# Kernel optimization log

Hardware: AMD Instinct MI355X
Metric: run time of the kernel (lower is better)

Reference implementation:

```python
import jax, jax.numpy as jnp
import numpy as np

B, T, C = 2, 4096, 2048
HS = 64
H = C // HS            # 32 heads
D_W, D_A, D_MV, D_G = 128, 128, 64, 224
EPS_GN = 0.00064
EPS_NORM = 1e-12


def setup_inputs() -> dict:
    key = jax.random.key(0)
    ks = jax.random.split(key, 24)
    n = lambda k, s, sc=1.0: (jax.random.normal(k, s, dtype=jnp.float32) * sc)
    inp = {
        "x": n(ks[0], (B, T, C)),
        "v_first": n(ks[1], (B, T, C)),
        "y": n(ks[2], (B, T, C)),
        # token-shift mixing coefficients [1,1,C]
        "x_r": n(ks[3], (1, 1, C), 0.1), "x_w": n(ks[4], (1, 1, C), 0.1),
        "x_k": n(ks[5], (1, 1, C), 0.1), "x_v": n(ks[6], (1, 1, C), 0.1),
        "x_a": n(ks[7], (1, 1, C), 0.1), "x_g": n(ks[8], (1, 1, C), 0.1),
        # decay LoRA
        "w0": n(ks[9], (1, 1, C), 0.5) - 3.0,
        "w1": n(ks[10], (C, D_W), 0.02), "w2": n(ks[11], (D_W, C), 0.02),
        # in-context-rate LoRA
        "a0": n(ks[12], (1, 1, C), 0.2),
        "a1": n(ks[13], (C, D_A), 0.02), "a2": n(ks[14], (D_A, C), 0.02),
        # value-mix LoRA
        "v0": n(ks[15], (1, 1, C), 0.2) + 0.73,
        "v1": n(ks[16], (C, D_MV), 0.02), "v2": n(ks[17], (D_MV, C), 0.02),
        # gate LoRA
        "g1": n(ks[18], (C, D_G), 0.02), "g2": n(ks[19], (D_G, C), 0.02),
        "k_k": jnp.full((1, 1, C), 0.71, dtype=jnp.float32),
        "k_a": jnp.full((1, 1, C), 1.02, dtype=jnp.float32),
        "r_k": jnp.full((H, HS), -0.04, dtype=jnp.float32),
        # square projections
        "W_r": n(ks[20], (C, C), 0.5 / C ** 0.5),
        "W_k": n(ks[21], (C, C), 0.05 / C ** 0.5),
        "W_v": n(ks[22], (C, C), 0.5 / C ** 0.5),
        "W_o": n(ks[23], (C, C), 0.02),
        "ln_g": jnp.ones((C,), dtype=jnp.float32),
        "ln_b": jnp.zeros((C,), dtype=jnp.float32),
    }
    return inp


def reference(x, v_first, y, x_r, x_w, x_k, x_v, x_a, x_g,
              w0, w1, w2, a0, a1, a2, v0, v1, v2, g1, g2,
              k_k, k_a, r_k, W_r, W_k, W_v, W_o, ln_g, ln_b):
    Bx, Tx, Cx = x.shape
    Hn, hs = r_k.shape

    # ---- project ----
    xx = jnp.pad(x[:, :-1, :], ((0, 0), (1, 0), (0, 0))) - x  # time_shift_1(x) - x
    xr = x + xx * x_r
    xw = x + xx * x_w
    xk = x + xx * x_k
    xv = x + xx * x_v
    xa = x + xx * x_a
    xg = x + xx * x_g

    r = xr @ W_r.T
    w = -jax.nn.softplus(-(w0 + jnp.tanh(xw @ w1) @ w2)) - 0.5
    k = xk @ W_k.T
    v = xv @ W_v.T
    # layer_id == 1 (> 0): mix with v_first
    v = v + (v_first - v) * jax.nn.sigmoid(v0 + (xv @ v1) @ v2)
    a = jax.nn.sigmoid(a0 + (xa @ a1) @ a2)
    g = jax.nn.sigmoid(xg @ g1) @ g2

    kk = k * k_k
    kkh = kk.reshape(Bx, Tx, Hn, hs)
    nrm = jnp.sqrt(jnp.sum(kkh * kkh, axis=-1, keepdims=True))
    kk = (kkh / jnp.maximum(nrm, EPS_NORM)).reshape(Bx, Tx, Cx)
    k = k * (1.0 + (a - 1.0) * k_a)

    # ---- post_kernel ----
    yh = y.reshape(Bx, Tx, Hn, hs)
    mu = jnp.mean(yh, axis=-1, keepdims=True)
    var = jnp.mean((yh - mu) ** 2, axis=-1, keepdims=True)
    yn = ((yh - mu) / jnp.sqrt(var + EPS_GN)).reshape(Bx, Tx, Cx)
    yn = yn * ln_g + ln_b

    rh = r.reshape(Bx, Tx, Hn, hs)
    kh = k.reshape(Bx, Tx, Hn, hs)
    vh = v.reshape(Bx, Tx, Hn, hs)
    dot = jnp.sum(rh * kh * r_k, axis=-1, keepdims=True)  # [B,T,H,1]
    y2 = yn + (dot * vh).reshape(Bx, Tx, Cx)
    out = (y2 * g) @ W_o.T
    return out, w, a, kk
```

## Files before the change

kernel.cpp:

```cpp
#include <hip/hip_runtime.h>
#include <math.h>

typedef unsigned short u16;
typedef __attribute__((ext_vector_type(8))) short short8;
typedef __attribute__((ext_vector_type(4))) float floatx4;
typedef __attribute__((ext_vector_type(4))) unsigned short ushort4v;
typedef __attribute__((ext_vector_type(8))) unsigned short ushort8v;

#define DEV static __device__ __forceinline__

DEV u16 f2b(float f) {
  unsigned u = __builtin_bit_cast(unsigned, f);
  u += 0x7fffu + ((u >> 16) & 1u);
  return (u16)(u >> 16);
}
DEV float b2f(u16 h) { return __builtin_bit_cast(float, ((unsigned)h) << 16); }

DEV void gld16(const u16* g, u16* l) {
  __builtin_amdgcn_global_load_lds((__attribute__((address_space(1))) void*)(g),
                                   (__attribute__((address_space(3))) void*)(l), 16, 0, 0);
}

__global__ __launch_bounds__(256) void ew_mix(
    const float* __restrict__ x,
    const float* __restrict__ cr, const float* __restrict__ ck,
    const float* __restrict__ cv, const float* __restrict__ cw,
    const float* __restrict__ ca, const float* __restrict__ cg,
    u16* __restrict__ oxr, u16* __restrict__ oxk, u16* __restrict__ oxv,
    u16* __restrict__ oxw, u16* __restrict__ oxa, u16* __restrict__ oxg)
{
  const long idx = (long)blockIdx.x * 256 + threadIdx.x;
  const long row = idx >> 8;
  const int c8 = (int)(idx & 255) << 3;
  const long off = (row << 11) + c8;
  const floatx4 xa_ = *(const floatx4*)(x + off);
  const floatx4 xb_ = *(const floatx4*)(x + off + 4);
  floatx4 pa = (floatx4)0.f, pb = (floatx4)0.f;
  if ((row & 4095) != 0) {
    pa = *(const floatx4*)(x + off - 2048);
    pb = *(const floatx4*)(x + off - 2044);
  }
  floatx4 da, db;
#pragma unroll
  for (int i = 0; i < 4; ++i) { da[i] = pa[i] - xa_[i]; db[i] = pb[i] - xb_[i]; }
#define EMIT(cp, op) {                                                         \
    const floatx4 c0 = *(const floatx4*)(cp + c8);                             \
    const floatx4 c1 = *(const floatx4*)(cp + c8 + 4);                         \
    ushort8v o;                                                                \
    _Pragma("unroll")                                                          \
    for (int i = 0; i < 4; ++i) {                                              \
      o[i]     = f2b(xa_[i] + da[i] * c0[i]);                                  \
      o[4 + i] = f2b(xb_[i] + db[i] * c1[i]);                                  \
    }                                                                          \
    *(ushort8v*)(op + off) = o; }
  EMIT(cr, oxr); EMIT(ck, oxk); EMIT(cv, oxv);
  EMIT(cw, oxw); EMIT(ca, oxa); EMIT(cg, oxg);
#undef EMIT
}

__global__ __launch_bounds__(256) void transpose_cast(
    const float* __restrict__ w1, const float* __restrict__ a1,
    const float* __restrict__ v1, const float* __restrict__ g1,
    const float* __restrict__ w2, const float* __restrict__ a2,
    const float* __restrict__ v2, const float* __restrict__ g2,
    u16* __restrict__ w1T, u16* __restrict__ a1T, u16* __restrict__ v1T,
    u16* __restrict__ g1T, u16* __restrict__ w2T, u16* __restrict__ a2T,
    u16* __restrict__ v2T, u16* __restrict__ g2T,
    const float* __restrict__ Wr, const float* __restrict__ Wk,
    const float* __restrict__ Wv, const float* __restrict__ Wo,
    u16* __restrict__ Wr16, u16* __restrict__ Wk16,
    u16* __restrict__ Wv16, u16* __restrict__ Wo16)
{
  const long idx = (long)blockIdx.x * 256 + threadIdx.x;
  if (blockIdx.y >= 8) {
    const float* s; u16* d;
    switch (blockIdx.y) {
      case 8:  s = Wr; d = Wr16; break;
      case 9:  s = Wk; d = Wk16; break;
      case 10: s = Wv; d = Wv16; break;
      default: s = Wo; d = Wo16; break;
    }
    const long i = idx * 8;
    const float4 a = *(const float4*)(s + i);
    const float4 b = *(const float4*)(s + i + 4);
    ushort4v lo = { f2b(a.x), f2b(a.y), f2b(a.z), f2b(a.w) };
    ushort4v hi = { f2b(b.x), f2b(b.y), f2b(b.z), f2b(b.w) };
    *(ushort4v*)(d + i) = lo;
    *(ushort4v*)(d + i + 4) = hi;
    return;
  }
  const float* src; u16* dst; int sk, sn, dn, dk;
  switch (blockIdx.y) {
    case 0: src = w1; dst = w1T; sk = 2048; sn = 128; dn = 128;  dk = 2048; break;
    case 1: src = a1; dst = a1T; sk = 2048; sn = 128; dn = 128;  dk = 2048; break;
    case 2: src = v1; dst = v1T; sk = 2048; sn = 64;  dn = 128;  dk = 2048; break;
    case 3: src = g1; dst = g1T; sk = 2048; sn = 224; dn = 256;  dk = 2048; break;
    case 4: src = w2; dst = w2T; sk = 128;  sn = 2048; dn = 2048; dk = 128; break;
    case 5: src = a2; dst = a2T; sk = 128;  sn = 2048; dn = 2048; dk = 128; break;
    case 6: src = v2; dst = v2T; sk = 64;   sn = 2048; dn = 2048; dk = 128; break;
    default:src = g2; dst = g2T; sk = 224;  sn = 2048; dn = 2048; dk = 256; break;
  }
  const long total = (long)dn * dk;
  if (idx >= total) return;
  const int n = (int)(idx / dk), k = (int)(idx % dk);
  float v = 0.f;
  if (k < sk && n < sn) v = src[(long)k * sn + n];
  dst[idx] = f2b(v);
}

#define GEMM128_BODY(Abase, Bbase, K)                                          \
  floatx4 acc[4][4];                                                           \
  _Pragma("unroll")                                                            \
  for (int i = 0; i < 4; ++i)                                                  \
    _Pragma("unroll")                                                          \
    for (int jq = 0; jq < 4; ++jq) acc[i][jq] = (floatx4)0.f;                  \
  const int nK = (K) >> 6;                                                     \
  for (int kt = 0; kt < nK; ++kt) {                                            \
    const int k0 = kt << 6;                                                    \
    __syncthreads();                                                           \
    _Pragma("unroll")                                                          \
    for (int i = 0; i < 4; ++i) {                                              \
      const int c = i * 256 + tid;                                             \
      const int row = c >> 3;                                                  \
      const int sch = (c & 7) ^ (row & 7);                                     \
      const long goff = (long)row * (K) + k0 + sch * 8;                        \
      const int lbase = (i * 256 + wave * 64) * 8;                             \
      gld16((Abase) + goff, &sA[lbase]);                                       \
      gld16((Bbase) + goff, &sB[lbase]);                                       \
    }                                                                          \
    asm volatile("s_waitcnt vmcnt(0)" ::: "memory");                           \
    __syncthreads();                                                           \
    _Pragma("unroll")                                                          \
    for (int ks = 0; ks < 2; ++ks) {                                           \
      short8 af[4], bfr[4];                                                    \
      _Pragma("unroll")                                                        \
      for (int mi = 0; mi < 4; ++mi) {                                         \
        const int row = wm * 64 + mi * 16 + lrow;                              \
        const int ch = (ks * 4 + lkg) ^ (row & 7);                             \
        af[mi] = *(const short8*)&sA[row * 64 + ch * 8];                       \
      }                                                                        \
      _Pragma("unroll")                                                        \
      for (int ni = 0; ni < 4; ++ni) {                                         \
        const int row = wn * 64 + ni * 16 + lrow;                              \
        const int ch = (ks * 4 + lkg) ^ (row & 7);                             \
        bfr[ni] = *(const short8*)&sB[row * 64 + ch * 8];                      \
      }                                                                        \
      _Pragma("unroll")                                                        \
      for (int mi = 0; mi < 4; ++mi)                                           \
        _Pragma("unroll")                                                      \
        for (int ni = 0; ni < 4; ++ni)                                         \
          acc[mi][ni] = __builtin_amdgcn_mfma_f32_16x16x32_bf16(af[mi], bfr[ni], acc[mi][ni], 0, 0, 0); \
    }                                                                          \
  }

__global__ __launch_bounds__(256, 2) void gemm_s1(
    const u16* __restrict__ xw, const u16* __restrict__ w1T, u16* __restrict__ hw,
    const u16* __restrict__ xa, const u16* __restrict__ a1T, u16* __restrict__ ha,
    const u16* __restrict__ xv, const u16* __restrict__ v1T, u16* __restrict__ hv,
    const u16* __restrict__ xg, const u16* __restrict__ g1T, u16* __restrict__ hg)
{
  __shared__ __align__(16) u16 sA[128 * 64];
  __shared__ __align__(16) u16 sB[128 * 64];
  const int bid = blockIdx.x;
  const int jid = (bid < 64) ? 0 : (bid < 128) ? 1 : (bid < 192) ? 2 : 3;
  const u16* A = (jid == 0) ? xw : (jid == 1) ? xa : (jid == 2) ? xv : xg;
  const u16* B = (jid == 0) ? w1T : (jid == 1) ? a1T : (jid == 2) ? v1T : g1T;
  u16* Cv = (jid == 0) ? hw : (jid == 1) ? ha : (jid == 2) ? hv : hg;
  const int N = (jid == 3) ? 256 : 128;
  const int lb = bid - ((jid == 0) ? 0 : (jid == 1) ? 64 : (jid == 2) ? 128 : 192);
  const int tid = threadIdx.x;
  const int wave = tid >> 6, lane = tid & 63;
  const int lrow = lane & 15, lkg = lane >> 4;
  const int wm = wave >> 1, wn = wave & 1;
  const int nbn = N >> 7;
  const int bm = lb / nbn, bn = lb % nbn;
  const u16* Abase = A + (long)bm * 128 * 2048;
  const u16* Bbase = B + (long)bn * 128 * 2048;

  GEMM128_BODY(Abase, Bbase, 2048)

  const int row0 = bm * 128 + wm * 64 + lkg * 4;
  const int col0 = bn * 128 + wn * 64 + lrow;
#pragma unroll
  for (int mi = 0; mi < 4; ++mi)
#pragma unroll
    for (int ni = 0; ni < 4; ++ni) {
      const int col = col0 + ni * 16;
#pragma unroll
      for (int r = 0; r < 4; ++r) {
        const long o = (long)(row0 + mi * 16 + r) * N + col;
        float v = acc[mi][ni][r];
        if (jid == 0) v = tanhf(v);
        else if (jid == 3) v = 1.f / (1.f + expf(-v));
        Cv[o] = f2b(v);
      }
    }
}

__global__ __launch_bounds__(256, 2) void gemm_s2(
    const u16* __restrict__ hw, const u16* __restrict__ w2T, float* __restrict__ wsec, const float* __restrict__ w0,
    const u16* __restrict__ ha, const u16* __restrict__ a2T, float* __restrict__ asec, const float* __restrict__ a0,
    const u16* __restrict__ hv, const u16* __restrict__ v2T, u16* __restrict__ vs, const float* __restrict__ v0,
    const u16* __restrict__ hg, const u16* __restrict__ g2T, u16* __restrict__ gb)
{
  __shared__ __align__(16) u16 sA[128 * 64];
  __shared__ __align__(16) u16 sB[128 * 64];
  const int jid = blockIdx.x >> 10;
  const int lb = blockIdx.x & 1023;
  const u16* A = (jid == 0) ? hw : (jid == 1) ? ha : (jid == 2) ? hv : hg;
  const u16* B = (jid == 0) ? w2T : (jid == 1) ? a2T : (jid == 2) ? v2T : g2T;
  const float* bias = (jid == 0) ? w0 : (jid == 1) ? a0 : v0;
  const int K = (jid == 3) ? 256 : 128;
  const int tid = threadIdx.x;
  const int wave = tid >> 6, lane = tid & 63;
  const int lrow = lane & 15, lkg = lane >> 4;
  const int wm = wave >> 1, wn = wave & 1;
  const int bm = lb >> 4, bn = lb & 15;
  const u16* Abase = A + (long)bm * 128 * K;
  const u16* Bbase = B + (long)bn * 128 * K;

  GEMM128_BODY(Abase, Bbase, K)

  const int row0 = bm * 128 + wm * 64 + lkg * 4;
  const int col0 = bn * 128 + wn * 64 + lrow;
#pragma unroll
  for (int mi = 0; mi < 4; ++mi)
#pragma unroll
    for (int ni = 0; ni < 4; ++ni) {
      const int col = col0 + ni * 16;
#pragma unroll
      for (int r = 0; r < 4; ++r) {
        const long o = (long)(row0 + mi * 16 + r) * 2048 + col;
        const float v = acc[mi][ni][r];
        if (jid == 0) {
          const float zz = -(v + bias[col]);
          const float sp = fmaxf(zz, 0.f) + log1pf(expf(-fabsf(zz)));
          wsec[o] = -sp - 0.5f;
        } else if (jid == 1) {
          asec[o] = 1.f / (1.f + expf(-(v + bias[col])));
        } else if (jid == 2) {
          vs[o] = f2b(1.f / (1.f + expf(-(v + bias[col]))));
        } else {
          gb[o] = f2b(v);
        }
      }
    }
}

template<int OP>
__global__ __launch_bounds__(512, 2) void gemm256(
    const u16* __restrict__ A0, const u16* __restrict__ B0, void* __restrict__ C0,
    const u16* __restrict__ A1, const u16* __restrict__ B1, void* __restrict__ C1,
    const u16* __restrict__ A2, const u16* __restrict__ B2, void* __restrict__ C2)
{
  __shared__ __align__(16) u16 lds[8 * 8192];
  const int tid = threadIdx.x;
  const int wave = tid >> 6, lane = tid & 63;
  const int lrow = lane & 15, lq = lane >> 4;
  const int wm = wave >> 2, wn = wave & 3;
  const int job = blockIdx.x >> 8;
  const int d = blockIdx.x & 255;
  const int lb = ((d & 7) << 5) | (d >> 3);
  const int bm = lb >> 3, bn = lb & 7;

  const u16* Aj = (job == 0) ? A0 : ((job == 1) ? A1 : A2);
  const u16* Bj = (job == 0) ? B0 : ((job == 1) ? B1 : B2);
  void* Cj      = (job == 0) ? C0 : ((job == 1) ? C1 : C2);

  const u16* __restrict__ Ab = Aj + (long)bm * 256 * 2048;
  const u16* __restrict__ Bb = Bj + (long)bn * 256 * 2048;

  int srco[2], dsto[2];
#pragma unroll
  for (int l = 0; l < 2; ++l) {
    const int c = l * 512 + tid;
    const int row = c >> 2, q = c & 3;
    const int qs = q ^ ((row >> 1) & 3);
    srco[l] = row * 2048 + qs * 8;
    dsto[l] = (l * 512 + wave * 64) * 8;
  }
  int offA[2][4], offB[4];
#pragma unroll
  for (int qm = 0; qm < 2; ++qm)
#pragma unroll
    for (int mi = 0; mi < 4; ++mi) {
      const int r = wm * 128 + qm * 64 + mi * 16 + lrow;
      offA[qm][mi] = r * 32 + (lq ^ ((r >> 1) & 3)) * 8;
    }
#pragma unroll
  for (int ni = 0; ni < 4; ++ni) {
    const int r = wn * 64 + ni * 16 + lrow;
    offB[ni] = r * 32 + (lq ^ ((r >> 1) & 3)) * 8;
  }

  floatx4 acc[8][4];
#pragma unroll
  for (int i = 0; i < 8; ++i)
#pragma unroll
    for (int jq = 0; jq < 4; ++jq) acc[i][jq] = (floatx4)0.f;

#define STAGE(sU, slot) {                                                  \
    const int t_ = (sU) >> 2, j_ = (sU) & 3;                               \
    const u16* base_ = (j_ & 1) ? Bb : Ab;                                 \
    const int kofs_ = t_ * 64 + ((j_ & 2) ? 32 : 0);                       \
    gld16(base_ + srco[0] + kofs_, &lds[(slot) * 8192 + dsto[0]]);         \
    gld16(base_ + srco[1] + kofs_, &lds[(slot) * 8192 + dsto[1]]);         \
  }

#pragma unroll
  for (int s = 0; s < 6; ++s) STAGE(s, s);
  asm volatile("s_waitcnt vmcnt(4)" ::: "memory");

#define SEC(P, sA_, sB_, sS0, sS1)                                             \
  {                                                                            \
    asm volatile("s_barrier" ::: "memory");                                    \
    if ((P) <= 60) {                                                           \
      STAGE(2 * (P) + 6, sS0);                                                 \
      STAGE(2 * (P) + 7, sS1);                                                 \
    }                                                                          \
    short8 af0[4], af1[4], bfv[4];                                             \
    _Pragma("unroll")                                                          \
    for (int mi = 0; mi < 4; ++mi)                                             \
      af0[mi] = *(const short8*)&lds[(sA_) * 8192 + offA[0][mi]];              \
    _Pragma("unroll")                                                          \
    for (int ni = 0; ni < 4; ++ni)                                             \
      bfv[ni] = *(const short8*)&lds[(sB_) * 8192 + offB[ni]];                 \
    _Pragma("unroll")                                                          \
    for (int mi = 0; mi < 4; ++mi)                                             \
      af1[mi] = *(const short8*)&lds[(sA_) * 8192 + offA[1][mi]];              \
    _Pragma("unroll")                                                          \
    for (int mi = 0; mi < 4; ++mi)                                             \
      _Pragma("unroll")                                                        \
      for (int ni = 0; ni < 4; ++ni)                                           \
        acc[mi][ni] = __builtin_amdgcn_mfma_f32_16x16x32_bf16(af0[mi], bfv[ni], acc[mi][ni], 0, 0, 0); \
    _Pragma("unroll")                                                          \
    for (int mi = 0; mi < 4; ++mi)                                             \
      _Pragma("unroll")                                                        \
      for (int ni = 0; ni < 4; ++ni)                                           \
        acc[4 + mi][ni] = __builtin_amdgcn_mfma_f32_16x16x32_bf16(af1[mi], bfv[ni], acc[4 + mi][ni], 0, 0, 0); \
    if ((P) < 62) { asm volatile("s_waitcnt vmcnt(4)" ::: "memory"); }         \
    else          { asm volatile("s_waitcnt vmcnt(0)" ::: "memory"); }         \
  }

  for (int pp = 0; pp < 64; pp += 4) {
    SEC(pp,     0, 1, 6, 7);
    SEC(pp + 1, 2, 3, 0, 1);
    SEC(pp + 2, 4, 5, 2, 3);
    SEC(pp + 3, 6, 7, 4, 5);
  }
#undef SEC
#undef STAGE

  const long row0 = (long)bm * 256 + wm * 128 + lq * 4;
  const int col0 = bn * 256 + wn * 64 + lrow;
#pragma unroll
  for (int mi = 0; mi < 8; ++mi) {
#pragma unroll
    for (int ni = 0; ni < 4; ++ni) {
      const int col = col0 + ni * 16;
#pragma unroll
      for (int r = 0; r < 4; ++r) {
        const long o = (row0 + mi * 16 + r) * 2048 + col;
        const float v = acc[mi][ni][r];
        if constexpr (OP == 0) ((float*)Cj)[o] = v;
        else ((u16*)Cj)[o] = f2b(v);
      }
    }
  }
}

DEV float wsum16(float v) {
  v += __shfl_xor(v, 1);  v += __shfl_xor(v, 2);
  v += __shfl_xor(v, 4);  v += __shfl_xor(v, 8);
  return v;
}

__global__ __launch_bounds__(256) void ew_head(
    const u16* __restrict__ r16, const u16* __restrict__ k16,
    float* __restrict__ kkout,
    const float* __restrict__ abuf,
    const u16* __restrict__ v0buf, const u16* __restrict__ vsbuf,
    const u16* __restrict__ gbuf,
    const float* __restrict__ y, const float* __restrict__ vfirst,
    const float* __restrict__ kkc, const float* __restrict__ kac,
    const float* __restrict__ rk, const float* __restrict__ lng,
    const float* __restrict__ lnb, u16* __restrict__ z)
{
  const int tid = threadIdx.x;
  const long gh = (long)blockIdx.x * 16 + (tid >> 4);
  const long m = gh >> 5;
  const int h = (int)(gh & 31);
  const int li = tid & 15;
  const int c = h * 64 + li * 4;
  const long off = (m << 11) + c;

  const ushort4v k0p = *(const ushort4v*)(k16 + off);
  const floatx4 av   = *(const floatx4*)(abuf + off);
  const floatx4 kkcv = *(const floatx4*)(kkc + c);
  const floatx4 kacv = *(const floatx4*)(kac + c);
  float k0[4], kf[4], kr[4];
  float ss = 0.f;
#pragma unroll
  for (int i = 0; i < 4; ++i) {
    k0[i] = b2f(k0p[i]);
    kf[i] = k0[i] * (1.f + (av[i] - 1.f) * kacv[i]);
    kr[i] = k0[i] * kkcv[i];
    ss += kr[i] * kr[i];
  }
  const float nrm = sqrtf(wsum16(ss));
  const float rn = 1.f / fmaxf(nrm, 1e-12f);
  floatx4 kkv;
#pragma unroll
  for (int i = 0; i < 4; ++i) kkv[i] = kr[i] * rn;
  *(floatx4*)(kkout + off) = kkv;

  const floatx4 yv = *(const floatx4*)(y + off);
  const float mu = wsum16(yv[0] + yv[1] + yv[2] + yv[3]) * 0.015625f;
  float dy[4], sv2 = 0.f;
#pragma unroll
  for (int i = 0; i < 4; ++i) { dy[i] = yv[i] - mu; sv2 += dy[i] * dy[i]; }
  const float var = wsum16(sv2) * 0.015625f;
  const float rs = rsqrtf(var + 0.00064f);
  const floatx4 lngv = *(const floatx4*)(lng + c);
  const floatx4 lnbv = *(const floatx4*)(lnb + c);
  float yn[4];
#pragma unroll
  for (int i = 0; i < 4; ++i) yn[i] = dy[i] * rs * lngv[i] + lnbv[i];

  const ushort4v rp = *(const ushort4v*)(r16 + off);
  const floatx4 rkv = *(const floatx4*)(rk + c);
  float dd = 0.f;
#pragma unroll
  for (int i = 0; i < 4; ++i) dd += b2f(rp[i]) * kf[i] * rkv[i];
  const float dot = wsum16(dd);

  const ushort4v v0p = *(const ushort4v*)(v0buf + off);
  const ushort4v vsp = *(const ushort4v*)(vsbuf + off);
  const floatx4 vfv  = *(const floatx4*)(vfirst + off);
  const ushort4v gp  = *(const ushort4v*)(gbuf + off);
  ushort4v zo;
#pragma unroll
  for (int i = 0; i < 4; ++i) {
    const float v0v = b2f(v0p[i]);
    const float vv = v0v + (vfv[i] - v0v) * b2f(vsp[i]);
    zo[i] = f2b((yn[i] + dot * vv) * b2f(gp[i]));
  }
  *(ushort4v*)(z + off) = zo;
}

extern "C" void kernel_launch(void* const* d_in, const int* in_sizes, int n_in,
                              void* d_out, int out_size, void* d_ws, size_t ws_size,
                              hipStream_t stream)
{
  (void)in_sizes; (void)out_size;
  if (n_in < 29) return;
  const int Mrows = 8192;
  const long C = 2048;
  const long MB_ = (long)Mrows * C;

  const float* x   = (const float*)d_in[0];
  const float* vf  = (const float*)d_in[1];
  const float* y   = (const float*)d_in[2];
  const float* x_r = (const float*)d_in[3];
  const float* x_w = (const float*)d_in[4];
  const float* x_k = (const float*)d_in[5];
  const float* x_v = (const float*)d_in[6];
  const float* x_a = (const float*)d_in[7];
  const float* x_g = (const float*)d_in[8];
  const float* w0  = (const float*)d_in[9];
  const float* w1  = (const float*)d_in[10];
  const float* w2  = (const float*)d_in[11];
  const float* a0  = (const float*)d_in[12];
  const float* a1  = (const float*)d_in[13];
  const float* a2  = (const float*)d_in[14];
  const float* v0  = (const float*)d_in[15];
  const float* v1  = (const float*)d_in[16];
  const float* v2  = (const float*)d_in[17];
  const float* g1  = (const float*)d_in[18];
  const float* g2  = (const float*)d_in[19];
  const float* k_k = (const float*)d_in[20];
  const float* k_a = (const float*)d_in[21];
  const float* r_k = (const float*)d_in[22];
  const float* W_r = (const float*)d_in[23];
  const float* W_k = (const float*)d_in[24];
  const float* W_v = (const float*)d_in[25];
  const float* W_o = (const float*)d_in[26];
  const float* lng = (const float*)d_in[27];
  const float* lnb = (const float*)d_in[28];

  float* out_sec = (float*)d_out;
  float* w_sec   = out_sec + MB_;
  float* a_sec   = w_sec + MB_;
  float* kk_sec  = a_sec + MB_;

  u16* k16 = (u16*)out_sec;
  u16* r16 = (u16*)out_sec + MB_;
  u16* Wr16 = (u16*)w_sec;
  u16* Wk16 = Wr16 + C * C;
  u16* Wv16 = Wk16 + C * C;

  u16* p = (u16*)d_ws;
  u16* xr = p;            p += MB_;
  u16* xk = p;            p += MB_;
  u16* xv = p;            p += MB_;
  u16* xw = p;            p += MB_;
  u16* xa = p;            p += MB_;
  u16* xg = p;            p += MB_;
  u16* Wo16 = p;          p += C * C;
  u16* w1T = p;           p += 128 * C;
  u16* a1T = p;           p += 128 * C;
  u16* v1T = p;           p += 128 * C;
  u16* g1T = p;           p += 256 * C;
  u16* w2T = p;           p += C * 128;
  u16* a2T = p;           p += C * 128;
  u16* v2T = p;           p += C * 128;
  u16* g2T = p;           p += C * 256;
  u16* hw  = p;           p += (long)Mrows * 128;
  u16* ha  = p;           p += (long)Mrows * 128;
  u16* hv  = p;           p += (long)Mrows * 128;
  u16* hg  = p;           p += (long)Mrows * 256;
  const size_t need = (size_t)((char*)p - (char*)d_ws);
  if (ws_size < need) return;

  u16* v0buf = xg;
  u16* zbuf  = xk;
  u16* vsbuf = xw;
  u16* gbuf  = xa;

  ew_mix<<<8192, 256, 0, stream>>>(x, x_r, x_k, x_v, x_w, x_a, x_g,
                                   xr, xk, xv, xw, xa, xg);
  transpose_cast<<<dim3(2048, 12), 256, 0, stream>>>(
      w1, a1, v1, g1, w2, a2, v2, g2,
      w1T, a1T, v1T, g1T, w2T, a2T, v2T, g2T,
      W_r, W_k, W_v, W_o, Wr16, Wk16, Wv16, Wo16);
  gemm_s1<<<320, 256, 0, stream>>>(xw, w1T, hw, xa, a1T, ha,
                                   xv, v1T, hv, xg, g1T, hg);
  gemm256<1><<<768, 512, 0, stream>>>(xr, Wr16, r16,
                                      xk, Wk16, k16,
                                      xv, Wv16, v0buf);
  gemm_s2<<<4096, 256, 0, stream>>>(hw, w2T, w_sec, w0,
                                    ha, a2T, a_sec, a0,
                                    hv, v2T, vsbuf, v0,
                                    hg, g2T, gbuf);
  ew_head<<<16384, 256, 0, stream>>>(r16, k16, kk_sec, a_sec, v0buf, vsbuf, gbuf,
                                     y, vf, k_k, k_a, r_k, lng, lnb, zbuf);
  gemm256<0><<<256, 512, 0, stream>>>(zbuf, Wo16, out_sec,
                                      zbuf, Wo16, out_sec,
                                      zbuf, Wo16, out_sec);
}
```

Measured before the change: 672.2 us.

## Fuse LoRA second-stage GEMMs with head elementwise epilogue into one kernel

Replaces the separate gemm_s2 kernel and the ew_head elementwise kernel with a single s2_head kernel. Each block runs the a, v, g and w LoRA up-projections for the same 128x128 output tile back to back, keeping a, the value-mix sigmoid and the gate in registers as packed bf16. It then does the key normalisation, group norm, r·k dot and z computation in place. This removes the global round trips for the vs and g intermediates and the re-read of a, plus one kernel launch. In exchange it raises register pressure from the extra packed tiles and cuts the grid from 4096 blocks to 1024. It also uses scalar, less vectorised loads in the epilogue.

Result: slower. 704.5 us (+4.8%).

```diff
diff --git a/kernel.cpp b/kernel.cpp
--- a/kernel.cpp
+++ b/kernel.cpp
@@ -110,46 +110,51 @@
 
 #define GEMM128_BODY(Abase, Bbase, K)                                          \
   floatx4 acc[4][4];                                                           \
+  GEMM128_RUN(Abase, Bbase, K)
+
+#define GEMM128_RUN(Abase, Bbase, K)                                           \
   _Pragma("unroll")                                                            \
   for (int i = 0; i < 4; ++i)                                                  \
     _Pragma("unroll")                                                          \
     for (int jq = 0; jq < 4; ++jq) acc[i][jq] = (floatx4)0.f;                  \
-  const int nK = (K) >> 6;                                                     \
-  for (int kt = 0; kt < nK; ++kt) {                                            \
-    const int k0 = kt << 6;                                                    \
-    __syncthreads();                                                           \
-    _Pragma("unroll")                                                          \
-    for (int i = 0; i < 4; ++i) {                                              \
-      const int c = i * 256 + tid;                                             \
-      const int row = c >> 3;                                                  \
-      const int sch = (c & 7) ^ (row & 7);                                     \
-      const long goff = (long)row * (K) + k0 + sch * 8;                        \
-      const int lbase = (i * 256 + wave * 64) * 8;                             \
-      gld16((Abase) + goff, &sA[lbase]);                                       \
-      gld16((Bbase) + goff, &sB[lbase]);                                       \
-    }                                                                          \
-    asm volatile("s_waitcnt vmcnt(0)" ::: "memory");                           \
-    __syncthreads();                                                           \
-    _Pragma("unroll")                                                          \
-    for (int ks = 0; ks < 2; ++ks) {                                           \
-      short8 af[4], bfr[4];                                                    \
+  {                                                                            \
+    const int nK = (K) >> 6;                                                   \
+    for (int kt = 0; kt < nK; ++kt) {                                          \
+      const int kk0 = kt << 6;                                                 \
+      __syncthreads();                                                         \
       _Pragma("unroll")                                                        \
-      for (int mi = 0; mi < 4; ++mi) {                                         \
-        const int row = wm * 64 + mi * 16 + lrow;                              \
-        const int ch = (ks * 4 + lkg) ^ (row & 7);                             \
-        af[mi] = *(const short8*)&sA[row * 64 + ch * 8];                       \
+      for (int i = 0; i < 4; ++i) {                                            \
+        const int c = i * 256 + tid;                                           \
+        const int row = c >> 3;                                                \
+        const int sch = (c & 7) ^ (row & 7);                                   \
+        const long goff = (long)row * (K) + kk0 + sch * 8;                     \
+        const int lbase = (i * 256 + wave * 64) * 8;                           \
+        gld16((Abase) + goff, &sA[lbase]);                                     \
+        gld16((Bbase) + goff, &sB[lbase]);                                     \
       }                                                                        \
+      asm volatile("s_waitcnt vmcnt(0)" ::: "memory");                         \
+      __syncthreads();                                                         \
       _Pragma("unroll")                                                        \
-      for (int ni = 0; ni < 4; ++ni) {                                         \
-        const int row = wn * 64 + ni * 16 + lrow;                              \
-        const int ch = (ks * 4 + lkg) ^ (row & 7);                             \
-        bfr[ni] = *(const short8*)&sB[row * 64 + ch * 8];                      \
+      for (int ks = 0; ks < 2; ++ks) {                                         \
+        short8 af[4], bfr[4];                                                  \
+        _Pragma("unroll")                                                      \
+        for (int mi = 0; mi < 4; ++mi) {                                       \
+          const int row = wm * 64 + mi * 16 + lrow;                            \
+          const int ch = (ks * 4 + lkg) ^ (row & 7);                           \
+          af[mi] = *(const short8*)&sA[row * 64 + ch * 8];                     \
+        }                                                                      \
+        _Pragma("unroll")                                                      \
+        for (int ni = 0; ni < 4; ++ni) {                                       \
+          const int row = wn * 64 + ni * 16 + lrow;                            \
+          const int ch = (ks * 4 + lkg) ^ (row & 7);                           \
+          bfr[ni] = *(const short8*)&sB[row * 64 + ch * 8];                    \
+        }                                                                      \
+        _Pragma("unroll")                                                      \
+        for (int mi = 0; mi < 4; ++mi)                                         \
+          _Pragma("unroll")                                                    \
+          for (int ni = 0; ni < 4; ++ni)                                       \
+            acc[mi][ni] = __builtin_amdgcn_mfma_f32_16x16x32_bf16(af[mi], bfr[ni], acc[mi][ni], 0, 0, 0); \
       }                                                                        \
-      _Pragma("unroll")                                                        \
-      for (int mi = 0; mi < 4; ++mi)                                           \
-        _Pragma("unroll")                                                      \
-        for (int ni = 0; ni < 4; ++ni)                                         \
-          acc[mi][ni] = __builtin_amdgcn_mfma_f32_16x16x32_bf16(af[mi], bfr[ni], acc[mi][ni], 0, 0, 0); \
     }                                                                          \
   }
 
@@ -197,54 +202,140 @@
     }
 }
 
-__global__ __launch_bounds__(256, 2) void gemm_s2(
-    const u16* __restrict__ hw, const u16* __restrict__ w2T, float* __restrict__ wsec, const float* __restrict__ w0,
-    const u16* __restrict__ ha, const u16* __restrict__ a2T, float* __restrict__ asec, const float* __restrict__ a0,
-    const u16* __restrict__ hv, const u16* __restrict__ v2T, u16* __restrict__ vs, const float* __restrict__ v0,
-    const u16* __restrict__ hg, const u16* __restrict__ g2T, u16* __restrict__ gb)
+__global__ __launch_bounds__(256, 2) void s2_head(
+    const u16* __restrict__ hw, const u16* __restrict__ w2T,
+    float* __restrict__ wsec, const float* __restrict__ w0,
+    const u16* __restrict__ ha, const u16* __restrict__ a2T,
+    float* __restrict__ asec, const float* __restrict__ a0,
+    const u16* __restrict__ hv, const u16* __restrict__ v2T,
+    const float* __restrict__ v0,
+    const u16* __restrict__ hg, const u16* __restrict__ g2T,
+    const u16* __restrict__ r16, const u16* __restrict__ k16,
+    const u16* __restrict__ v0buf,
+    const float* __restrict__ y, const float* __restrict__ vfirst,
+    const float* __restrict__ kkc, const float* __restrict__ kac,
+    const float* __restrict__ rk, const float* __restrict__ lng,
+    const float* __restrict__ lnb,
+    float* __restrict__ kkout, u16* __restrict__ z)
 {
   __shared__ __align__(16) u16 sA[128 * 64];
   __shared__ __align__(16) u16 sB[128 * 64];
-  const int jid = blockIdx.x >> 10;
-  const int lb = blockIdx.x & 1023;
-  const u16* A = (jid == 0) ? hw : (jid == 1) ? ha : (jid == 2) ? hv : hg;
-  const u16* B = (jid == 0) ? w2T : (jid == 1) ? a2T : (jid == 2) ? v2T : g2T;
-  const float* bias = (jid == 0) ? w0 : (jid == 1) ? a0 : v0;
-  const int K = (jid == 3) ? 256 : 128;
   const int tid = threadIdx.x;
   const int wave = tid >> 6, lane = tid & 63;
   const int lrow = lane & 15, lkg = lane >> 4;
   const int wm = wave >> 1, wn = wave & 1;
-  const int bm = lb >> 4, bn = lb & 15;
-  const u16* Abase = A + (long)bm * 128 * K;
-  const u16* Bbase = B + (long)bn * 128 * K;
-
-  GEMM128_BODY(Abase, Bbase, K)
+  const int bm = blockIdx.x >> 4, bn = blockIdx.x & 15;
 
   const int row0 = bm * 128 + wm * 64 + lkg * 4;
   const int col0 = bn * 128 + wn * 64 + lrow;
-#pragma unroll
-  for (int mi = 0; mi < 4; ++mi)
-#pragma unroll
-    for (int ni = 0; ni < 4; ++ni) {
-      const int col = col0 + ni * 16;
+
+  floatx4 acc[4][4];
+  ushort4v aPk[4][4], vPk[4][4], gPk[4][4];
+
+  GEMM128_RUN(ha + (long)bm * 128 * 128, a2T + (long)bn * 128 * 128, 128)
+#pragma unroll
+  for (int ni = 0; ni < 4; ++ni) {
+    const float bias = a0[col0 + ni * 16];
+#pragma unroll
+    for (int mi = 0; mi < 4; ++mi)
 #pragma unroll
       for (int r = 0; r < 4; ++r) {
-        const long o = (long)(row0 + mi * 16 + r) * 2048 + col;
-        const float v = acc[mi][ni][r];
-        if (jid == 0) {
-          const float zz = -(v + bias[col]);
-          const float sp = fmaxf(zz, 0.f) + log1pf(expf(-fabsf(zz)));
-          wsec[o] = -sp - 0.5f;
-        } else if (jid == 1) {
-          asec[o] = 1.f / (1.f + expf(-(v + bias[col])));
-        } else if (jid == 2) {
-          vs[o] = f2b(1.f / (1.f + expf(-(v + bias[col]))));
-        } else {
-          gb[o] = f2b(v);
-        }
+        const float v = 1.f / (1.f + expf(-(acc[mi][ni][r] + bias)));
+        asec[(long)(row0 + mi * 16 + r) * 2048 + col0 + ni * 16] = v;
+        aPk[mi][ni][r] = f2b(v);
+      }
+  }
+  GEMM128_RUN(hv + (long)bm * 128 * 128, v2T + (long)bn * 128 * 128, 128)
+#pragma unroll
+  for (int ni = 0; ni < 4; ++ni) {
+    const float bias = v0[col0 + ni * 16];
+#pragma unroll
+    for (int mi = 0; mi < 4; ++mi)
+#pragma unroll
+      for (int r = 0; r < 4; ++r)
+        vPk[mi][ni][r] = f2b(1.f / (1.f + expf(-(acc[mi][ni][r] + bias))));
+  }
+  GEMM128_RUN(hg + (long)bm * 128 * 256, g2T + (long)bn * 128 * 256, 256)
+#pragma unroll
+  for (int ni = 0; ni < 4; ++ni)
+#pragma unroll
+    for (int mi = 0; mi < 4; ++mi)
+#pragma unroll
+      for (int r = 0; r < 4; ++r)
+        gPk[mi][ni][r] = f2b(acc[mi][ni][r]);
+  GEMM128_RUN(hw + (long)bm * 128 * 128, w2T + (long)bn * 128 * 128, 128)
+#pragma unroll
+  for (int ni = 0; ni < 4; ++ni) {
+    const float bias = w0[col0 + ni * 16];
+#pragma unroll
+    for (int mi = 0; mi < 4; ++mi)
+#pragma unroll
+      for (int r = 0; r < 4; ++r) {
+        const float zz = -(acc[mi][ni][r] + bias);
+        const float sp = fmaxf(zz, 0.f) + log1pf(expf(-fabsf(zz)));
+        wsec[(long)(row0 + mi * 16 + r) * 2048 + col0 + ni * 16] = -sp - 0.5f;
+      }
+  }
+
+  float kkcv[4], kacv[4], rkv[4], lngv[4], lnbv[4];
+#pragma unroll
+  for (int ni = 0; ni < 4; ++ni) {
+    const int c = col0 + ni * 16;
+    kkcv[ni] = kkc[c]; kacv[ni] = kac[c]; rkv[ni] = rk[c];
+    lngv[ni] = lng[c]; lnbv[ni] = lnb[c];
+  }
+#pragma unroll
+  for (int mi = 0; mi < 4; ++mi) {
+#pragma unroll
+    for (int r = 0; r < 4; ++r) {
+      const long rowoff = (long)(row0 + mi * 16 + r) * 2048 + col0;
+      float k0v[4], rv[4], yv[4], vfv[4], v0v[4];
+#pragma unroll
+      for (int ni = 0; ni < 4; ++ni) {
+        const long off = rowoff + ni * 16;
+        k0v[ni] = b2f(k16[off]);
+        rv[ni]  = b2f(r16[off]);
+        yv[ni]  = y[off];
+        vfv[ni] = vfirst[off];
+        v0v[ni] = b2f(v0buf[off]);
+      }
+      float ss = 0.f, sy = 0.f;
+#pragma unroll
+      for (int ni = 0; ni < 4; ++ni) {
+        const float kr = k0v[ni] * kkcv[ni];
+        ss += kr * kr; sy += yv[ni];
+      }
+      ss += __shfl_xor(ss, 1); ss += __shfl_xor(ss, 2);
+      ss += __shfl_xor(ss, 4); ss += __shfl_xor(ss, 8);
+      sy += __shfl_xor(sy, 1); sy += __shfl_xor(sy, 2);
+      sy += __shfl_xor(sy, 4); sy += __shfl_xor(sy, 8);
+      const float rn = 1.f / fmaxf(sqrtf(ss), 1e-12f);
+      const float mu = sy * 0.015625f;
+      float sv = 0.f, dd = 0.f;
+#pragma unroll
+      for (int ni = 0; ni < 4; ++ni) {
+        const float dy = yv[ni] - mu;
+        sv += dy * dy;
+        const float av = b2f(aPk[mi][ni][r]);
+        const float kf = k0v[ni] * (1.f + (av - 1.f) * kacv[ni]);
+        dd += rv[ni] * kf * rkv[ni];
+      }
+      sv += __shfl_xor(sv, 1); sv += __shfl_xor(sv, 2);
+      sv += __shfl_xor(sv, 4); sv += __shfl_xor(sv, 8);
+      dd += __shfl_xor(dd, 1); dd += __shfl_xor(dd, 2);
+      dd += __shfl_xor(dd, 4); dd += __shfl_xor(dd, 8);
+      const float rs = rsqrtf(sv * 0.015625f + 0.00064f);
+#pragma unroll
+      for (int ni = 0; ni < 4; ++ni) {
+        const long off = rowoff + ni * 16;
+        kkout[off] = k0v[ni] * kkcv[ni] * rn;
+        const float yn = (yv[ni] - mu) * rs * lngv[ni] + lnbv[ni];
+        const float v0x = v0v[ni];
+        const float vv = v0x + (vfv[ni] - v0x) * b2f(vPk[mi][ni][r]);
+        z[off] = f2b((yn + dd * vv) * b2f(gPk[mi][ni][r]));
       }
     }
+  }
 }
 
 template<int OP>
@@ -367,85 +458,6 @@
       }
     }
   }
-}
-
-DEV float wsum16(float v) {
-  v += __shfl_xor(v, 1);  v += __shfl_xor(v, 2);
-  v += __shfl_xor(v, 4);  v += __shfl_xor(v, 8);
-  return v;
-}
-
-__global__ __launch_bounds__(256) void ew_head(
-    const u16* __restrict__ r16, const u16* __restrict__ k16,
-    float* __restrict__ kkout,
-    const float* __restrict__ abuf,
-    const u16* __restrict__ v0buf, const u16* __restrict__ vsbuf,
-    const u16* __restrict__ gbuf,
-    const float* __restrict__ y, const float* __restrict__ vfirst,
-    const float* __restrict__ kkc, const float* __restrict__ kac,
-    const float* __restrict__ rk, const float* __restrict__ lng,
-    const float* __restrict__ lnb, u16* __restrict__ z)
-{
-  const int tid = threadIdx.x;
-  const long gh = (long)blockIdx.x * 16 + (tid >> 4);
-  const long m = gh >> 5;
-  const int h = (int)(gh & 31);
-  const int li = tid & 15;
-  const int c = h * 64 + li * 4;
-  const long off = (m << 11) + c;
-
-  const ushort4v k0p = *(const ushort4v*)(k16 + off);
-  const floatx4 av   = *(const floatx4*)(abuf + off);
-  const floatx4 kkcv = *(const floatx4*)(kkc + c);
-  const floatx4 kacv = *(const floatx4*)(kac + c);
-  float k0[4], kf[4], kr[4];
-  float ss = 0.f;
-#pragma unroll
-  for (int i = 0; i < 4; ++i) {
-    k0[i] = b2f(k0p[i]);
-    kf[i] = k0[i] * (1.f + (av[i] - 1.f) * kacv[i]);
-    kr[i] = k0[i] * kkcv[i];
-    ss += kr[i] * kr[i];
-  }
-  const float nrm = sqrtf(wsum16(ss));
-  const float rn = 1.f / fmaxf(nrm, 1e-12f);
-  floatx4 kkv;
-#pragma unroll
-  for (int i = 0; i < 4; ++i) kkv[i] = kr[i] * rn;
-  *(floatx4*)(kkout + off) = kkv;
-
-  const floatx4 yv = *(const floatx4*)(y + off);
-  const float mu = wsum16(yv[0] + yv[1] + yv[2] + yv[3]) * 0.015625f;
-  float dy[4], sv2 = 0.f;
-#pragma unroll
-  for (int i = 0; i < 4; ++i) { dy[i] = yv[i] - mu; sv2 += dy[i] * dy[i]; }
-  const float var = wsum16(sv2) * 0.015625f;
-  const float rs = rsqrtf(var + 0.00064f);
-  const floatx4 lngv = *(const floatx4*)(lng + c);
-  const floatx4 lnbv = *(const floatx4*)(lnb + c);
-  float yn[4];
-#pragma unroll
-  for (int i = 0; i < 4; ++i) yn[i] = dy[i] * rs * lngv[i] + lnbv[i];
-
-  const ushort4v rp = *(const ushort4v*)(r16 + off);
-  const floatx4 rkv = *(const floatx4*)(rk + c);
-  float dd = 0.f;
-#pragma unroll
-  for (int i = 0; i < 4; ++i) dd += b2f(rp[i]) * kf[i] * rkv[i];
-  const float dot = wsum16(dd);
-
-  const ushort4v v0p = *(const ushort4v*)(v0buf + off);
-  const ushort4v vsp = *(const ushort4v*)(vsbuf + off);
-  const floatx4 vfv  = *(const floatx4*)(vfirst + off);
-  const ushort4v gp  = *(const ushort4v*)(gbuf + off);
-  ushort4v zo;
-#pragma unroll
-  for (int i = 0; i < 4; ++i) {
-    const float v0v = b2f(v0p[i]);
-    const float vv = v0v + (vfv[i] - v0v) * b2f(vsp[i]);
-    zo[i] = f2b((yn[i] + dot * vv) * b2f(gp[i]));
-  }
-  *(ushort4v*)(z + off) = zo;
 }
 
 extern "C" void kernel_launch(void* const* d_in, const int* in_sizes, int n_in,
@@ -524,8 +536,6 @@
 
   u16* v0buf = xg;
   u16* zbuf  = xk;
-  u16* vsbuf = xw;
-  u16* gbuf  = xa;
 
   ew_mix<<<8192, 256, 0, stream>>>(x, x_r, x_k, x_v, x_w, x_a, x_g,
                                    xr, xk, xv, xw, xa, xg);
@@ -538,12 +548,13 @@
   gemm256<1><<<768, 512, 0, stream>>>(xr, Wr16, r16,
                                       xk, Wk16, k16,
                                       xv, Wv16, v0buf);
-  gemm_s2<<<4096, 256, 0, stream>>>(hw, w2T, w_sec, w0,
+  s2_head<<<1024, 256, 0, stream>>>(hw, w2T, w_sec, w0,
                                     ha, a2T, a_sec, a0,
-                                    hv, v2T, vsbuf, v0,
-                                    hg, g2T, gbuf);
-  ew_head<<<16384, 256, 0, stream>>>(r16, k16, kk_sec, a_sec, v0buf, vsbuf, gbuf,
-                                     y, vf, k_k, k_a, r_k, lng, lnb, zbuf);
+                                    hv, v2T, v0,
+                                    hg, g2T,
+                                    r16, k16, v0buf, y, vf,
+                                    k_k, k_a, r_k, lng, lnb,
+                                    kk_sec, zbuf);
   gemm256<0><<<256, 512, 0, stream>>>(zbuf, Wo16, out_sec,
                                       zbuf, Wo16, out_sec,
                                       zbuf, Wo16, out_sec);
```
